# Optimization experiments

Measured on AMD Instinct MI355X. Metric: run time of the kernel, lower is better.

## Reference

```python
import jax, jax.numpy as jnp
import numpy as np

N = 100000
C = 128
H = 8
D = C // H  # head_dim = 16
E = 640000


def setup_inputs() -> dict:
    key = jax.random.key(0)
    ks = jax.random.split(key, 10)
    s = 1.0 / np.sqrt(C)
    return {
        "features": jax.random.normal(ks[0], (N, C), dtype=jnp.float32),
        "edge_index": jax.random.randint(ks[1], (2, E), 0, N, dtype=jnp.int64),
        "Wq": jax.random.uniform(ks[2], (C, C), jnp.float32, -s, s),
        "bq": jnp.zeros((C,), jnp.float32),
        "Wk": jax.random.uniform(ks[3], (C, C), jnp.float32, -s, s),
        "bk": jnp.zeros((C,), jnp.float32),
        "Wv": jax.random.uniform(ks[4], (C, C), jnp.float32, -s, s),
        "bv": jnp.zeros((C,), jnp.float32),
        "Wo": jax.random.uniform(ks[5], (C, C), jnp.float32, -s, s),
        "bo": jnp.zeros((C,), jnp.float32),
    }


def reference(features, edge_index, Wq, bq, Wk, bk, Wv, bv, Wo, bo):
    row, col = edge_index[0], edge_index[1]  # [E], [E]
    # Linear projections (torch Linear: x @ W.T + b), reshape to heads
    q = (features @ Wq.T + bq).reshape(N, H, D)
    k = (features @ Wk.T + bk).reshape(N, H, D)
    v = (features @ Wv.T + bv).reshape(N, H, D)
    # Per-edge dot-product scores [E, H]
    attn = jnp.einsum('ehd,ehd->eh', q[row], k[col]) / jnp.sqrt(jnp.float32(D))
    # Faithful to original: softmax over ALL edges (dim=0), per head
    attn = jax.nn.softmax(attn, axis=0)
    # Weighted scatter-add of source values into destination nodes
    msgs = attn[:, :, None] * v[col]  # [E, H, D]
    out = jax.ops.segment_sum(msgs, row, num_segments=N)  # [N, H, D]
    out = out.reshape(N, C)
    return out @ Wo.T + bo
```

## Files before the change

kernel.cpp:

```cpp
#include <hip/hip_runtime.h>


#define TPB 256

typedef __attribute__((ext_vector_type(8))) short short8;
typedef __attribute__((ext_vector_type(4))) short short4v;
typedef __attribute__((ext_vector_type(4))) float f32x4;

__device__ __forceinline__ short f2bf(float f) {
    unsigned u = __float_as_uint(f);
    u += 0x7fffu + ((u >> 16) & 1u);
    return (short)(u >> 16);
}
__device__ __forceinline__ float bf2f(short s) {
    return __uint_as_float(((unsigned)(unsigned short)s) << 16);
}

template<bool IN_BF16, bool OUT_BF16>
__device__ __forceinline__ void gemm_body(
    const void* __restrict__ Xv, int nrows,
    const short* __restrict__ Wb, const float* __restrict__ bias,
    void* __restrict__ Yv, int xblk)
{
    __shared__ short lw[16384];
    const int tid = threadIdx.x;

    short8 wreg[8];
    #pragma unroll
    for (int r = 0; r < 8; ++r) {
        int c = r * 256 + tid;
        int fragid = c >> 6, ln = c & 63;
        int n = fragid >> 2, kc = fragid & 3;
        wreg[r] = *(const short8*)&Wb[(n*16 + (ln & 15))*128 + kc*32 + (ln >> 4)*8];
    }

    const int wid = tid >> 6;
    const int lane = tid & 63;
    const int l15 = lane & 15;
    const int lh  = lane >> 4;
    const int rowbase = xblk * 128 + wid * 32;
    const int r0 = rowbase + l15, r1 = r0 + 16;
    const bool vv0 = r0 < nrows, vv1 = r1 < nrows;

    short8 xfr[4][2];
    if (IN_BF16) {
        const short* Xb = (const short*)Xv;
        #pragma unroll
        for (int kc = 0; kc < 4; ++kc) {
            xfr[kc][0] = vv0 ? *(const short8*)&Xb[(size_t)r0*128 + kc*32 + lh*8]
                             : (short8)(short)0;
            xfr[kc][1] = vv1 ? *(const short8*)&Xb[(size_t)r1*128 + kc*32 + lh*8]
                             : (short8)(short)0;
        }
    } else {
        const float* Xf = (const float*)Xv;
        const float4* P0 = (const float4*)(Xf + (size_t)r0 * 128);
        const float4* P1 = (const float4*)(Xf + (size_t)r1 * 128);
        float4 xa[4][2], xb[4][2];
        #pragma unroll
        for (int kc = 0; kc < 4; ++kc) {
            xa[kc][0] = vv0 ? P0[kc*8 + lh*2]     : make_float4(0.f,0.f,0.f,0.f);
            xb[kc][0] = vv0 ? P0[kc*8 + lh*2 + 1] : make_float4(0.f,0.f,0.f,0.f);
            xa[kc][1] = vv1 ? P1[kc*8 + lh*2]     : make_float4(0.f,0.f,0.f,0.f);
            xb[kc][1] = vv1 ? P1[kc*8 + lh*2 + 1] : make_float4(0.f,0.f,0.f,0.f);
        }
        #pragma unroll
        for (int kc = 0; kc < 4; ++kc)
            #pragma unroll
            for (int g = 0; g < 2; ++g) {
                xfr[kc][g][0] = f2bf(xa[kc][g].x);
                xfr[kc][g][1] = f2bf(xa[kc][g].y);
                xfr[kc][g][2] = f2bf(xa[kc][g].z);
                xfr[kc][g][3] = f2bf(xa[kc][g].w);
                xfr[kc][g][4] = f2bf(xb[kc][g].x);
                xfr[kc][g][5] = f2bf(xb[kc][g].y);
                xfr[kc][g][6] = f2bf(xb[kc][g].z);
                xfr[kc][g][7] = f2bf(xb[kc][g].w);
            }
    }

    #pragma unroll
    for (int r = 0; r < 8; ++r)
        *(short8*)&lw[(r * 256 + tid) * 8] = wreg[r];
    __syncthreads();

    f32x4 acc[8][2];
    #pragma unroll
    for (int n = 0; n < 8; ++n) { acc[n][0] = (f32x4)0.f; acc[n][1] = (f32x4)0.f; }

    #pragma unroll
    for (int kc = 0; kc < 4; ++kc) {
        short8 wf[8];
        #pragma unroll
        for (int n = 0; n < 8; ++n)
            wf[n] = *(const short8*)&lw[((n*4 + kc)*64 + lane) * 8];
        #pragma unroll
        for (int n = 0; n < 8; ++n) {
            acc[n][0] = __builtin_amdgcn_mfma_f32_16x16x32_bf16(wf[n], xfr[kc][0], acc[n][0], 0, 0, 0);
            acc[n][1] = __builtin_amdgcn_mfma_f32_16x16x32_bf16(wf[n], xfr[kc][1], acc[n][1], 0, 0, 0);
        }
    }

    #pragma unroll
    for (int g = 0; g < 2; ++g) {
        int row = rowbase + g*16 + l15;
        if (row >= nrows) continue;
        #pragma unroll
        for (int n = 0; n < 8; ++n) {
            float4 b4 = *(const float4*)&bias[n*16 + lh*4];
            float y0 = acc[n][g][0] + b4.x;
            float y1 = acc[n][g][1] + b4.y;
            float y2 = acc[n][g][2] + b4.z;
            float y3 = acc[n][g][3] + b4.w;
            if (OUT_BF16) {
                short4v s; s[0]=f2bf(y0); s[1]=f2bf(y1); s[2]=f2bf(y2); s[3]=f2bf(y3);
                *(short4v*)&((short*)Yv)[(size_t)row * 128 + n*16 + lh*4] = s;
            } else {
                *(float4*)&((float*)Yv)[(size_t)row * 128 + n*16 + lh*4] =
                    make_float4(y0, y1, y2, y3);
            }
        }
    }
}

__global__ __launch_bounds__(256) void gemm_out_kernel(
    const short* __restrict__ Xb, int nrows,
    const short* __restrict__ Wb, const float* __restrict__ bias,
    float* __restrict__ Y)
{
    gemm_body<true, false>(Xb, nrows, Wb, bias, Y, blockIdx.x);
}

__global__ __launch_bounds__(256) void gemm_qkv_kernel(
    const float* __restrict__ X, int nrows, int nxblk,
    const short* __restrict__ WB,
    const float* __restrict__ bq, const float* __restrict__ bk,
    const float* __restrict__ bv,
    short* __restrict__ Yb, size_t slice)
{
    int b = blockIdx.x;
    int k = b & 7, j = b >> 3;
    int jd = j / 3, w = j - 3 * jd;
    int x = k + 8 * jd;
    if (x >= nxblk) return;
    const float* bias = (w == 0) ? bq : (w == 1) ? bk : bv;
    gemm_body<false, true>(X, nrows, WB + w * 16384, bias,
                           Yb + (size_t)w * slice, x);
}

__global__ void init_kernel(int* __restrict__ deg, int n,
                            const int* __restrict__ raw, int* __restrict__ flag)
{
    int i = blockIdx.x * TPB + threadIdx.x;
    if (i < n) deg[i] = 0;
    if (blockIdx.x == 0 && threadIdx.x == 0) {
        int odd_nonzero = 0;
        for (int k = 0; k < 128; ++k)
            if (raw[2 * k + 1] != 0) odd_nonzero = 1;
        *flag = odd_nonzero ? 0 : 1;
    }
}

__global__ void conv_hist_wconv_kernel(
    const void* __restrict__ raw, int E, const int* __restrict__ flag,
    int* __restrict__ out, int* __restrict__ deg, int ebC,
    const float* __restrict__ W0, const float* __restrict__ W1,
    const float* __restrict__ W2, const float* __restrict__ W3,
    short* __restrict__ WB)
{
    int b = blockIdx.x;
    if (b < ebC) {
        int i = b * TPB + threadIdx.x;
        if (i >= 2 * E) return;
        int v;
        if (*flag) v = (int)((const long long*)raw)[i];
        else       v = ((const int*)raw)[i];
        out[i] = v;
        if (i < E) atomicAdd(&deg[v], 1);
    } else {
        int i = (b - ebC) * TPB + threadIdx.x;
        if (i >= 65536) return;
        const float* W = (i < 16384) ? W0 : (i < 32768) ? W1 : (i < 49152) ? W2 : W3;
        WB[i] = f2bf(W[i & 16383]);
    }
}

__global__ void scan1_kernel(const int* __restrict__ deg, int n,
                             int* __restrict__ rowstart, int* __restrict__ bsum)
{
    __shared__ int sm[TPB];
    int t = threadIdx.x;
    int gid = blockIdx.x * TPB + t;
    int v = (gid < n) ? deg[gid] : 0;
    sm[t] = v;
    __syncthreads();
    for (int off = 1; off < TPB; off <<= 1) {
        int x = (t >= off) ? sm[t - off] : 0;
        __syncthreads();
        sm[t] += x;
        __syncthreads();
    }
    if (gid < n) rowstart[gid] = sm[t] - v;
    if (t == TPB - 1) bsum[blockIdx.x] = sm[t];
}

__global__ void scan2_kernel(int* __restrict__ bsum, int nb)
{
    __shared__ int sm[512];
    int t = threadIdx.x;
    int v = (t < nb) ? bsum[t] : 0;
    sm[t] = v;
    __syncthreads();
    for (int off = 1; off < 512; off <<= 1) {
        int x = (t >= off) ? sm[t - off] : 0;
        __syncthreads();
        sm[t] += x;
        __syncthreads();
    }
    if (t < nb) bsum[t] = sm[t] - v;
}

__global__ void scan3_kernel(int* __restrict__ rowstart, int* __restrict__ cursor,
                             int n, int E, const int* __restrict__ bsum)
{
    int gid = blockIdx.x * TPB + threadIdx.x;
    if (gid < n) {
        int v = rowstart[gid] + bsum[blockIdx.x];
        rowstart[gid] = v;
        cursor[gid] = v;
    }
    if (gid == 0) rowstart[n] = E;
}

__global__ void fill_kernel(const int* __restrict__ ei, int E,
                            int* __restrict__ cursor, int* __restrict__ ecol)
{
    int e = blockIdx.x * TPB + threadIdx.x;
    if (e >= E) return;
    int pos = atomicAdd(&cursor[ei[e]], 1);
    ecol[pos] = ei[E + e];
}

__global__ __launch_bounds__(256) void csr_score_stats_kernel(
    const short* __restrict__ Qb, const short* __restrict__ Kb,
    const int* __restrict__ ecol, const int* __restrict__ rowstart, int N,
    float* __restrict__ S, float* __restrict__ mpart, float* __restrict__ zpart)
{
    int t = threadIdx.x;
    int idx = blockIdx.x * TPB + t;
    float m = -3.0e38f, z = 0.f;
    if (idx < N * 8) {
        int node = idx >> 3, h = idx & 7;
        const short8* q8 = (const short8*)(Qb + (size_t)node * 128 + h * 16);
        short8 q0 = q8[0], q1 = q8[1];
        int p0 = rowstart[node], p1 = rowstart[node + 1];
        if (p0 < p1) {
            short8 ka0, ka1, kb0, kb1;
            {
                const short8* kp = (const short8*)(Kb + (size_t)ecol[p0] * 128 + h * 16);
                ka0 = kp[0]; ka1 = kp[1];
            }
            if (p0 + 1 < p1) {
                const short8* kp = (const short8*)(Kb + (size_t)ecol[p0+1] * 128 + h * 16);
                kb0 = kp[0]; kb1 = kp[1];
            } else { kb0 = ka0; kb1 = ka1; }

            for (int p = p0; p < p1; ++p) {
                short8 kc0 = kb0, kc1 = kb1;
                if (p + 2 < p1) {
                    const short8* kp = (const short8*)(Kb + (size_t)ecol[p+2] * 128 + h * 16);
                    kc0 = kp[0]; kc1 = kp[1];
                }
                float dot = 0.f;
                #pragma unroll
                for (int i = 0; i < 8; ++i) {
                    dot += bf2f(q0[i]) * bf2f(ka0[i]);
                    dot += bf2f(q1[i]) * bf2f(ka1[i]);
                }
                float s = dot * 0.25f;
                S[(size_t)p * 8 + h] = s;
                float M = fmaxf(m, s);
                z = z * __expf(m - M) + __expf(s - M);
                m = M;
                ka0 = kb0; ka1 = kb1; kb0 = kc0; kb1 = kc1;
            }
        }
    }
    __shared__ float sm[TPB], sz[TPB];
    sm[t] = m; sz[t] = z;
    __syncthreads();
    for (int off = 128; off >= 8; off >>= 1) {
        if (t < off) {
            float m2 = sm[t + off], z2 = sz[t + off];
            float M = fmaxf(sm[t], m2);
            sz[t] = sz[t] * __expf(sm[t] - M) + z2 * __expf(m2 - M);
            sm[t] = M;
        }
        __syncthreads();
    }
    if (t < 8) {
        mpart[blockIdx.x * 8 + t] = sm[t];
        zpart[blockIdx.x * 8 + t] = sz[t];
    }
}

__global__ void stats_reduce_kernel(const float* __restrict__ mpart,
                                    const float* __restrict__ zpart,
                                    int nb, float* __restrict__ MZ)
{
    int t = threadIdx.x;
    int h = t & 7, chunk = t >> 3;
    float m = -3.0e38f, z = 0.f;
    for (int i = chunk; i < nb; i += 32) {
        float m2 = mpart[i * 8 + h], z2 = zpart[i * 8 + h];
        float M = fmaxf(m, m2);
        z = z * __expf(m - M) + z2 * __expf(m2 - M);
        m = M;
    }
    __shared__ float sm[TPB], sz[TPB];
    sm[t] = m; sz[t] = z;
    __syncthreads();
    for (int off = 128; off >= 8; off >>= 1) {
        if (t < off) {
            float m2 = sm[t + off], z2 = sz[t + off];
            float M = fmaxf(sm[t], m2);
            sz[t] = sz[t] * __expf(sm[t] - M) + z2 * __expf(m2 - M);
            sm[t] = M;
        }
        __syncthreads();
    }
    if (t < 8) { MZ[t] = sm[t]; MZ[8 + t] = sz[t]; }
}

__global__ __launch_bounds__(256) void gather_kernel(
    const float* __restrict__ S, const short* __restrict__ Vb,
    const int* __restrict__ ecol,
    const int* __restrict__ rowstart,
    const float* __restrict__ MZ, int N,
    short* __restrict__ outb)
{
    int idx = blockIdx.x * TPB + threadIdx.x;
    if (idx >= N * 8) return;
    int node = idx >> 3, h = idx & 7;
    float M = MZ[h];
    float invZ = 1.0f / MZ[8 + h];
    int p0 = rowstart[node], p1 = rowstart[node + 1];

    float a[16];
    #pragma unroll
    for (int i = 0; i < 16; ++i) a[i] = 0.f;

    if (p0 < p1) {
        short8 va0, va1, vb0, vb1;
        float sa, sb;
        {
            const short8* vp = (const short8*)(Vb + (size_t)ecol[p0] * 128 + h * 16);
            va0 = vp[0]; va1 = vp[1];
            sa = S[(size_t)p0 * 8 + h];
        }
        if (p0 + 1 < p1) {
            const short8* vp = (const short8*)(Vb + (size_t)ecol[p0+1] * 128 + h * 16);
            vb0 = vp[0]; vb1 = vp[1];
            sb = S[(size_t)(p0+1) * 8 + h];
        } else { vb0 = va0; vb1 = va1; sb = sa; }

        for (int p = p0; p < p1; ++p) {
            short8 vc0 = vb0, vc1 = vb1;
            float sc = sb;
            if (p + 2 < p1) {
                const short8* vp = (const short8*)(Vb + (size_t)ecol[p+2] * 128 + h * 16);
                vc0 = vp[0]; vc1 = vp[1];
                sc = S[(size_t)(p+2) * 8 + h];
            }
            float w = __expf(sa - M) * invZ;
            #pragma unroll
            for (int i = 0; i < 8; ++i) {
                a[i]     += w * bf2f(va0[i]);
                a[8 + i] += w * bf2f(va1[i]);
            }
            va0 = vb0; va1 = vb1; vb0 = vc0; vb1 = vc1;
            sa = sb; sb = sc;
        }
    }
    short8 o0, o1;
    #pragma unroll
    for (int i = 0; i < 8; ++i) { o0[i] = f2bf(a[i]); o1[i] = f2bf(a[8 + i]); }
    short8* ob = (short8*)(outb + (size_t)node * 128 + h * 16);
    ob[0] = o0; ob[1] = o1;
}

extern "C" void kernel_launch(void* const* d_in, const int* in_sizes, int n_in,
                              void* d_out, int out_size, void* d_ws, size_t ws_size,
                              hipStream_t stream)
{
    const float* feat = (const float*)d_in[0];
    const void*  eraw = d_in[1];
    const float* Wq = (const float*)d_in[2];
    const float* bq = (const float*)d_in[3];
    const float* Wk = (const float*)d_in[4];
    const float* bk = (const float*)d_in[5];
    const float* Wv = (const float*)d_in[6];
    const float* bv = (const float*)d_in[7];
    const float* Wo = (const float*)d_in[8];
    const float* bo = (const float*)d_in[9];

    const int N = in_sizes[0] / 128;
    const int E = in_sizes[1] / 2;
    const size_t NC = (size_t)N * 128;
    const int EH = E * 8;
    const int gbN = (N * 8 + TPB - 1) / TPB;

    short* Qb   = (short*)d_ws;
    short* Kb   = Qb + NC;
    short* Vb   = Kb + NC;
    short* ACCb = Vb + NC;
    float* S    = (float*)(ACCb + NC);
    int*   EI   = (int*)(S + EH);
    short* WB   = (short*)(EI + 2 * E);
    float* mpart = (float*)(WB + 65536);
    float* zpart = mpart + (size_t)gbN * 8;
    float* MZ    = zpart + (size_t)gbN * 8;
    int*   flag  = (int*)(MZ + 16);
    int* deg      = flag + 16;
    int* rowstart = deg + N;
    int* cursor   = rowstart + N + 1;
    int* bsum     = cursor + N;
    int* ecol     = bsum + 512;

    const int nbS = (N + TPB - 1) / TPB;
    const int ebE = (E + TPB - 1) / TPB;
    const int ebC = (2 * E + TPB - 1) / TPB;

    init_kernel<<<nbS, TPB, 0, stream>>>(deg, N, (const int*)eraw, flag);
    conv_hist_wconv_kernel<<<ebC + 256, TPB, 0, stream>>>(
        eraw, E, flag, EI, deg, ebC, Wq, Wk, Wv, Wo, WB);
    scan1_kernel<<<nbS, TPB, 0, stream>>>(deg, N, rowstart, bsum);
    scan2_kernel<<<1, 512, 0, stream>>>(bsum, nbS);
    scan3_kernel<<<nbS, TPB, 0, stream>>>(rowstart, cursor, N, E, bsum);
    fill_kernel<<<ebE, TPB, 0, stream>>>(EI, E, cursor, ecol);

    const int gb = (N + 127) / 128;
    const int qkvgrid = 8 * 3 * ((gb + 7) / 8);
    gemm_qkv_kernel<<<qkvgrid, TPB, 0, stream>>>(feat, N, gb, WB, bq, bk, bv, Qb, NC);

    csr_score_stats_kernel<<<gbN, TPB, 0, stream>>>(Qb, Kb, ecol, rowstart, N,
                                                    S, mpart, zpart);
    stats_reduce_kernel<<<1, TPB, 0, stream>>>(mpart, zpart, gbN, MZ);

    gather_kernel<<<gbN, TPB, 0, stream>>>(S, Vb, ecol, rowstart, MZ, N, ACCb);

    gemm_out_kernel<<<gb, TPB, 0, stream>>>(ACCb, N, WB + 3 * 16384, bo, (float*)d_out);
}
```

Measured before the change: 254.5 us.

## Parallelize score and softmax-stats kernel over edges instead of CSR rows

The fill kernel now also writes a sorted per-edge row array, and the score/stats kernel switches from one thread per (node, head) walking its CSR row to a grid-stride loop over (edge, head) pairs with a fixed grid of 2500 blocks. This removes load imbalance from varying node degree and the serial per-row dependency chain. In exchange, Q rows are re-read per edge instead of once per node, and the fill kernel does an extra scattered write.

```diff
diff --git a/kernel.cpp b/kernel.cpp
--- a/kernel.cpp
+++ b/kernel.cpp
@@ -233,58 +233,42 @@
 }
 
 __global__ void fill_kernel(const int* __restrict__ ei, int E,
-                            int* __restrict__ cursor, int* __restrict__ ecol)
+                            int* __restrict__ cursor,
+                            int* __restrict__ ecol, int* __restrict__ erow)
 {
     int e = blockIdx.x * TPB + threadIdx.x;
     if (e >= E) return;
-    int pos = atomicAdd(&cursor[ei[e]], 1);
+    int r = ei[e];
+    int pos = atomicAdd(&cursor[r], 1);
     ecol[pos] = ei[E + e];
-}
-
-__global__ __launch_bounds__(256) void csr_score_stats_kernel(
+    erow[pos] = r;
+}
+
+__global__ __launch_bounds__(256) void epar_score_stats_kernel(
     const short* __restrict__ Qb, const short* __restrict__ Kb,
-    const int* __restrict__ ecol, const int* __restrict__ rowstart, int N,
+    const int* __restrict__ erow, const int* __restrict__ ecol, int EH,
     float* __restrict__ S, float* __restrict__ mpart, float* __restrict__ zpart)
 {
     int t = threadIdx.x;
-    int idx = blockIdx.x * TPB + t;
+    int stride = gridDim.x * TPB;
     float m = -3.0e38f, z = 0.f;
-    if (idx < N * 8) {
-        int node = idx >> 3, h = idx & 7;
-        const short8* q8 = (const short8*)(Qb + (size_t)node * 128 + h * 16);
-        short8 q0 = q8[0], q1 = q8[1];
-        int p0 = rowstart[node], p1 = rowstart[node + 1];
-        if (p0 < p1) {
-            short8 ka0, ka1, kb0, kb1;
-            {
-                const short8* kp = (const short8*)(Kb + (size_t)ecol[p0] * 128 + h * 16);
-                ka0 = kp[0]; ka1 = kp[1];
-            }
-            if (p0 + 1 < p1) {
-                const short8* kp = (const short8*)(Kb + (size_t)ecol[p0+1] * 128 + h * 16);
-                kb0 = kp[0]; kb1 = kp[1];
-            } else { kb0 = ka0; kb1 = ka1; }
-
-            for (int p = p0; p < p1; ++p) {
-                short8 kc0 = kb0, kc1 = kb1;
-                if (p + 2 < p1) {
-                    const short8* kp = (const short8*)(Kb + (size_t)ecol[p+2] * 128 + h * 16);
-                    kc0 = kp[0]; kc1 = kp[1];
-                }
-                float dot = 0.f;
-                #pragma unroll
-                for (int i = 0; i < 8; ++i) {
-                    dot += bf2f(q0[i]) * bf2f(ka0[i]);
-                    dot += bf2f(q1[i]) * bf2f(ka1[i]);
-                }
-                float s = dot * 0.25f;
-                S[(size_t)p * 8 + h] = s;
-                float M = fmaxf(m, s);
-                z = z * __expf(m - M) + __expf(s - M);
-                m = M;
-                ka0 = kb0; ka1 = kb1; kb0 = kc0; kb1 = kc1;
-            }
-        }
+    for (int idx = blockIdx.x * TPB + t; idx < EH; idx += stride) {
+        int p = idx >> 3, h = idx & 7;
+        int r = erow[p], c = ecol[p];
+        const short8* q8 = (const short8*)(Qb + (size_t)r * 128 + h * 16);
+        const short8* k8 = (const short8*)(Kb + (size_t)c * 128 + h * 16);
+        short8 q0 = q8[0], q1 = q8[1], k0 = k8[0], k1 = k8[1];
+        float dot = 0.f;
+        #pragma unroll
+        for (int i = 0; i < 8; ++i) {
+            dot += bf2f(q0[i]) * bf2f(k0[i]);
+            dot += bf2f(q1[i]) * bf2f(k1[i]);
+        }
+        float s = dot * 0.25f;
+        S[idx] = s;
+        float M = fmaxf(m, s);
+        z = z * __expf(m - M) + __expf(s - M);
+        m = M;
     }
     __shared__ float sm[TPB], sz[TPB];
     sm[t] = m; sz[t] = z;
@@ -409,6 +393,7 @@
     const size_t NC = (size_t)N * 128;
     const int EH = E * 8;
     const int gbN = (N * 8 + TPB - 1) / TPB;
+    const int EG  = 2500;
 
     short* Qb   = (short*)d_ws;
     short* Kb   = Qb + NC;
@@ -418,14 +403,15 @@
     int*   EI   = (int*)(S + EH);
     short* WB   = (short*)(EI + 2 * E);
     float* mpart = (float*)(WB + 65536);
-    float* zpart = mpart + (size_t)gbN * 8;
-    float* MZ    = zpart + (size_t)gbN * 8;
+    float* zpart = mpart + (size_t)EG * 8;
+    float* MZ    = zpart + (size_t)EG * 8;
     int*   flag  = (int*)(MZ + 16);
     int* deg      = flag + 16;
     int* rowstart = deg + N;
     int* cursor   = rowstart + N + 1;
     int* bsum     = cursor + N;
     int* ecol     = bsum + 512;
+    int* erow     = ecol + E;
 
     const int nbS = (N + TPB - 1) / TPB;
     const int ebE = (E + TPB - 1) / TPB;
@@ -437,15 +423,15 @@
     scan1_kernel<<<nbS, TPB, 0, stream>>>(deg, N, rowstart, bsum);
     scan2_kernel<<<1, 512, 0, stream>>>(bsum, nbS);
     scan3_kernel<<<nbS, TPB, 0, stream>>>(rowstart, cursor, N, E, bsum);
-    fill_kernel<<<ebE, TPB, 0, stream>>>(EI, E, cursor, ecol);
+    fill_kernel<<<ebE, TPB, 0, stream>>>(EI, E, cursor, ecol, erow);
 
     const int gb = (N + 127) / 128;
     const int qkvgrid = 8 * 3 * ((gb + 7) / 8);
     gemm_qkv_kernel<<<qkvgrid, TPB, 0, stream>>>(feat, N, gb, WB, bq, bk, bv, Qb, NC);
 
-    csr_score_stats_kernel<<<gbN, TPB, 0, stream>>>(Qb, Kb, ecol, rowstart, N,
+    epar_score_stats_kernel<<<EG, TPB, 0, stream>>>(Qb, Kb, erow, ecol, EH,
                                                     S, mpart, zpart);
-    stats_reduce_kernel<<<1, TPB, 0, stream>>>(mpart, zpart, gbN, MZ);
+    stats_reduce_kernel<<<1, TPB, 0, stream>>>(mpart, zpart, EG, MZ);
 
     gather_kernel<<<gbN, TPB, 0, stream>>>(S, Vb, ecol, rowstart, MZ, N, ACCb);
 
```

Result: no change. 250.9 us (-1.4%).
